# Kernel optimization log

Hardware: AMD Instinct MI355X
Metric: run time of the kernel (lower is better)

## Reference

```python
import jax, jax.numpy as jnp
import numpy as np

B, TK, H = 32, 1024, 512
N = 2 * H          # hidden_dim * 2
AD = 512           # attention_dimension


def setup_inputs() -> dict:
    key = jax.random.key(0)
    ks = jax.random.split(key, 11)
    s = 0.02  # weight scale
    return {
        's_t_hat': jax.random.normal(ks[0], (B, N), jnp.float32),
        'encoder_outputs': jax.random.normal(ks[1], (B, TK, N), jnp.float32),
        'encoder_feature': jax.random.normal(ks[2], (B * TK, N), jnp.float32),
        'enc_padding_mask': jax.random.uniform(ks[3], (B, TK), jnp.float32),
        'coverage': jax.random.uniform(ks[4], (B, TK), jnp.float32),
        'r_i': jax.random.normal(ks[5], (B, TK, AD), jnp.float32),
        'W_s_w': jax.random.normal(ks[6], (N, N), jnp.float32) * s,
        'W_s_b': jax.random.normal(ks[7], (N,), jnp.float32) * s,
        'W_c_w': jax.random.normal(ks[8], (N, 1), jnp.float32) * s,
        'v_w': jax.random.normal(ks[9], (1, N), jnp.float32) * s,
        'W_r_w': jax.random.normal(ks[10], (N, AD), jnp.float32) * s,
    }


def reference(s_t_hat, encoder_outputs, encoder_feature, enc_padding_mask,
              coverage, r_i, W_s_w, W_s_b, W_c_w, v_w, W_r_w):
    b, t_k, n = encoder_outputs.shape
    # decoder feature: W_s(s_t_hat), broadcast over time
    dec_fea = s_t_hat @ W_s_w.T + W_s_b                       # [b, n]
    enc_feat = encoder_feature.reshape(b, t_k, n)             # [b, t_k, n]
    # coverage feature: W_c applied to scalar coverage per position
    cov_feat = coverage[..., None] * W_c_w[:, 0]              # [b, t_k, n]
    e = jnp.tanh(enc_feat + dec_fea[:, None, :] + cov_feat)   # [b, t_k, n]
    scores = jnp.einsum('btn,n->bt', e, v_w[0])               # [b, t_k]
    attn_ = jax.nn.softmax(scores, axis=1) * enc_padding_mask
    attn = attn_ / attn_.sum(1, keepdims=True)                # renormalized
    c_t = jnp.einsum('bt,btn->bn', attn, encoder_outputs)     # [b, n]
    coverage_new = coverage + attn                            # [b, t_k]
    # structural (LSA) branch
    Wrri = jnp.einsum('bta,na->btn', r_i, W_r_w)              # [b, t_k, n]
    e_s = jnp.tanh(Wrri + dec_fea[:, None, :])
    s2 = jnp.einsum('btn,n->bt', e_s, v_w[0])
    a_struct = (jax.nn.softmax(s2, axis=1) * enc_padding_mask)[:, None, :]  # [b,1,t_k]
    c_t_struct = jnp.einsum('bt,btn->bn', a_struct[:, 0], encoder_outputs)  # [b, n]
    return (c_t, attn, coverage_new, c_t_struct, a_struct)
```

## Files before the change

### kernel.cpp

```cpp
#include <hip/hip_runtime.h>
#include <hip/hip_bf16.h>

static constexpr int BB   = 32;
static constexpr int TKK  = 1024;
static constexpr int ND   = 1024;
static constexpr int ADIM = 512;

typedef __attribute__((ext_vector_type(8))) short bf16x8;
typedef __attribute__((ext_vector_type(4))) float f32x4;

__device__ __forceinline__ float fast_tanh(float x) {
  x = fminf(fmaxf(x, -15.f), 15.f);
  float e = __expf(2.f * x);
  return __fdividef(e - 1.f, e + 1.f);
}

__device__ __forceinline__ short f2bf(float x) {
  unsigned u = __float_as_uint(x);
  u += 0x7FFF + ((u >> 16) & 1);
  return (short)(u >> 16);
}

__device__ __forceinline__ void gload_lds16(const void* g, void* l) {
  __builtin_amdgcn_global_load_lds(
      (const __attribute__((address_space(1))) unsigned int*)g,
      (__attribute__((address_space(3))) unsigned int*)l, 16, 0, 0);
}

__global__ __launch_bounds__(256) void k_cvt2(const float* __restrict__ r_i,
    const float* __restrict__ Wr, short* __restrict__ rb, short* __restrict__ wb) {
  size_t bid = blockIdx.x;
  const float* src;
  short* dst;
  size_t i;
  if (bid < 8192) { src = r_i; dst = rb; i = bid * 256 + threadIdx.x; }
  else            { src = Wr;  dst = wb; i = (bid - 8192) * 256 + threadIdx.x; }
  float4 a = ((const float4*)src)[2 * i];
  float4 b = ((const float4*)src)[2 * i + 1];
  bf16x8 h;
  h[0] = f2bf(a.x); h[1] = f2bf(a.y); h[2] = f2bf(a.z); h[3] = f2bf(a.w);
  h[4] = f2bf(b.x); h[5] = f2bf(b.y); h[6] = f2bf(b.z); h[7] = f2bf(b.w);
  ((bf16x8*)dst)[i] = h;
}

__global__ __launch_bounds__(256) void k_decfea(const float* __restrict__ s_t_hat,
    const float* __restrict__ Wsw, const float* __restrict__ Wsb,
    float* __restrict__ dec) {
  int b  = blockIdx.x >> 3;
  int n0 = (blockIdx.x & 7) << 7;
  int w = threadIdx.x >> 6, lane = threadIdx.x & 63;
  const float4* s4 = (const float4*)(s_t_hat + (size_t)b * ND);
  float4 sv0 = s4[lane], sv1 = s4[lane + 64], sv2 = s4[lane + 128], sv3 = s4[lane + 192];
  for (int nn = 0; nn < 32; nn++) {
    int n = n0 + w * 32 + nn;
    const float4* w4 = (const float4*)(Wsw + (size_t)n * ND);
    float4 wa = w4[lane], wb = w4[lane + 64], wc = w4[lane + 128], wd = w4[lane + 192];
    float acc = sv0.x*wa.x + sv0.y*wa.y + sv0.z*wa.z + sv0.w*wa.w
              + sv1.x*wb.x + sv1.y*wb.y + sv1.z*wb.z + sv1.w*wb.w
              + sv2.x*wc.x + sv2.y*wc.y + sv2.z*wc.z + sv2.w*wc.w
              + sv3.x*wd.x + sv3.y*wd.y + sv3.z*wd.z + sv3.w*wd.w;
    #pragma unroll
    for (int off = 32; off; off >>= 1) acc += __shfl_down(acc, off);
    if (lane == 0) dec[b * ND + n] = acc + Wsb[n];
  }
}

__global__ __launch_bounds__(256) void k_scoresA(const float* __restrict__ ef,
    const float* __restrict__ dec, const float* __restrict__ Wc,
    const float* __restrict__ vw, const float* __restrict__ cov,
    float* __restrict__ scores) {
  __shared__ float sb[4];
  int bt = blockIdx.x;
  int b  = bt >> 10;
  int tid = threadIdx.x;
  float4 e = *(const float4*)(ef + (size_t)bt * ND + tid * 4);
  float4 d = *(const float4*)(dec + (size_t)b * ND + tid * 4);
  float4 w = *(const float4*)(Wc + tid * 4);
  float4 v = *(const float4*)(vw + tid * 4);
  float c = cov[bt];
  float s = v.x * fast_tanh(e.x + d.x + c * w.x)
          + v.y * fast_tanh(e.y + d.y + c * w.y)
          + v.z * fast_tanh(e.z + d.z + c * w.z)
          + v.w * fast_tanh(e.w + d.w + c * w.w);
  #pragma unroll
  for (int off = 32; off; off >>= 1) s += __shfl_down(s, off);
  if ((tid & 63) == 0) sb[tid >> 6] = s;
  __syncthreads();
  if (tid == 0) scores[bt] = sb[0] + sb[1] + sb[2] + sb[3];
}

__global__ __launch_bounds__(256) void k_softmaxA(const float* __restrict__ scores,
    const float* __restrict__ mask, const float* __restrict__ cov,
    float* __restrict__ attn, float* __restrict__ covnew) {
  __shared__ float sb[4];
  int b = blockIdx.x, tid = threadIdx.x;
  float4 s = *(const float4*)(scores + (size_t)b * TKK + tid * 4);
  float m = fmaxf(fmaxf(s.x, s.y), fmaxf(s.z, s.w));
  #pragma unroll
  for (int off = 32; off; off >>= 1) m = fmaxf(m, __shfl_down(m, off));
  if ((tid & 63) == 0) sb[tid >> 6] = m;
  __syncthreads();
  m = fmaxf(fmaxf(sb[0], sb[1]), fmaxf(sb[2], sb[3]));
  float4 mk = *(const float4*)(mask + (size_t)b * TKK + tid * 4);
  float4 e;
  e.x = __expf(s.x - m) * mk.x;
  e.y = __expf(s.y - m) * mk.y;
  e.z = __expf(s.z - m) * mk.z;
  e.w = __expf(s.w - m) * mk.w;
  float sum = e.x + e.y + e.z + e.w;
  #pragma unroll
  for (int off = 32; off; off >>= 1) sum += __shfl_down(sum, off);
  __syncthreads();
  if ((tid & 63) == 0) sb[tid >> 6] = sum;
  __syncthreads();
  float inv = __fdividef(1.f, sb[0] + sb[1] + sb[2] + sb[3]);
  float4 a = {e.x * inv, e.y * inv, e.z * inv, e.w * inv};
  *(float4*)(attn + (size_t)b * TKK + tid * 4) = a;
  float4 c = *(const float4*)(cov + (size_t)b * TKK + tid * 4);
  float4 cn = {c.x + a.x, c.y + a.y, c.z + a.z, c.w + a.w};
  *(float4*)(covnew + (size_t)b * TKK + tid * 4) = cn;
}

__global__ __launch_bounds__(256) void k_gemmB3(const short* __restrict__ rb,
    const short* __restrict__ wb, const float* __restrict__ dec,
    const float* __restrict__ vw, float* __restrict__ part) {
  __shared__ __align__(16) short As[2][128 * 32];
  __shared__ __align__(16) short Bs[2][128 * 32];
  const int tid = threadIdx.x;
  const int lane = tid & 63, wv = tid >> 6;
  const int wm = wv >> 1, wn = wv & 1;
  const int g = lane >> 4, cl = lane & 15;
  const int mchunk = blockIdx.x, nchunk = blockIdx.y;
  const int b  = mchunk >> 3;
  const int t0 = (mchunk & 7) * 128;
  const int n0 = nchunk * 128;
  const int lrow4 = lane >> 2;
  const int sck   = ((lane & 3) ^ ((lane >> 3) & 3)) * 8;
  const short* Agbase = rb + (size_t)(b * TKK + t0) * ADIM;
  const short* Bgbase = wb + (size_t)n0 * ADIM;
  const int rdsw = (g ^ ((cl >> 1) & 3)) * 8;

  f32x4 acc[4][4];
  #pragma unroll
  for (int m = 0; m < 4; ++m)
    #pragma unroll
    for (int n = 0; n < 4; ++n) acc[m][n] = (f32x4){0.f, 0.f, 0.f, 0.f};

  auto stage = [&](int buf, int kc) {
    const int k0 = kc * 32;
    #pragma unroll
    for (int p = 0; p < 2; ++p) {
      const int rowc = p * 64 + wv * 16;
      const int row  = rowc + lrow4;
      gload_lds16(Agbase + (size_t)row * ADIM + k0 + sck, &As[buf][rowc * 32]);
      gload_lds16(Bgbase + (size_t)row * ADIM + k0 + sck, &Bs[buf][rowc * 32]);
    }
  };

  stage(0, 0);
  for (int kc = 0; kc < 16; ++kc) {
    const int cur = kc & 1;
    if (kc < 15) {
      stage(cur ^ 1, kc + 1);
      asm volatile("s_waitcnt vmcnt(4)" ::: "memory");
    } else {
      asm volatile("s_waitcnt vmcnt(0)" ::: "memory");
    }
    __builtin_amdgcn_s_barrier();
    bf16x8 af[4], bfr[4];
    #pragma unroll
    for (int m = 0; m < 4; ++m)
      af[m] = *(const bf16x8*)&As[cur][(wm * 64 + m * 16 + cl) * 32 + rdsw];
    #pragma unroll
    for (int n = 0; n < 4; ++n)
      bfr[n] = *(const bf16x8*)&Bs[cur][(wn * 64 + n * 16 + cl) * 32 + rdsw];
    #pragma unroll
    for (int m = 0; m < 4; ++m)
      #pragma unroll
      for (int n = 0; n < 4; ++n)
        acc[m][n] = __builtin_amdgcn_mfma_f32_16x16x32_bf16(af[m], bfr[n], acc[m][n], 0, 0, 0);
    __builtin_amdgcn_s_barrier();
  }

  float vvv[4], ddd[4];
  #pragma unroll
  for (int n = 0; n < 4; ++n) {
    const int col = n0 + wn * 64 + n * 16 + cl;
    vvv[n] = vw[col];
    ddd[n] = dec[b * ND + col];
  }
  #pragma unroll
  for (int m = 0; m < 4; ++m) {
    #pragma unroll
    for (int r = 0; r < 4; ++r) {
      float s = 0.f;
      #pragma unroll
      for (int n = 0; n < 4; ++n)
        s += vvv[n] * fast_tanh(acc[m][n][r] + ddd[n]);
      #pragma unroll
      for (int off = 1; off < 16; off <<= 1) s += __shfl_xor(s, off);
      if (cl == 0) {
        const int rowg = b * TKK + t0 + wm * 64 + m * 16 + g * 4 + r;
        part[(size_t)rowg * 16 + nchunk * 2 + wn] = s;
      }
    }
  }
}

__global__ __launch_bounds__(256) void k_gemmB(const float* __restrict__ r_i,
    const float* __restrict__ Wr, const float* __restrict__ dec,
    const float* __restrict__ vw, float* __restrict__ part) {
  __shared__ short As[128 * 64];
  __shared__ short Bs[128 * 64];
  const int tid = threadIdx.x;
  const int lane = tid & 63, wv = tid >> 6;
  const int wm = wv >> 1, wn = wv & 1;
  const int g = lane >> 4, cl = lane & 15;
  const int mchunk = blockIdx.x, nchunk = blockIdx.y;
  const int b  = mchunk >> 3;
  const int t0 = (mchunk & 7) * 128;
  const int n0 = nchunk * 128;
  const float* Ag = r_i + (size_t)(b * TKK + t0) * ADIM;
  const float* Bg = Wr + (size_t)n0 * ADIM;
  const int srow = tid >> 3, skk = (tid & 7) * 8;

  f32x4 acc[4][4];
  #pragma unroll
  for (int m = 0; m < 4; ++m)
    #pragma unroll
    for (int n = 0; n < 4; ++n) acc[m][n] = (f32x4){0.f, 0.f, 0.f, 0.f};

  for (int kc = 0; kc < 8; ++kc) {
    const int k0 = kc * 64;
    __syncthreads();
    #pragma unroll
    for (int dit = 0; dit < 4; ++dit) {
      const int row = dit * 32 + srow;
      const float* sa = Ag + (size_t)row * ADIM + k0 + skk;
      float4 a0 = *(const float4*)sa, a1 = *(const float4*)(sa + 4);
      bf16x8 ha;
      ha[0]=f2bf(a0.x); ha[1]=f2bf(a0.y); ha[2]=f2bf(a0.z); ha[3]=f2bf(a0.w);
      ha[4]=f2bf(a1.x); ha[5]=f2bf(a1.y); ha[6]=f2bf(a1.z); ha[7]=f2bf(a1.w);
      *(bf16x8*)&As[row * 64 + skk] = ha;
      const float* sbp = Bg + (size_t)row * ADIM + k0 + skk;
      float4 b0 = *(const float4*)sbp, b1 = *(const float4*)(sbp + 4);
      bf16x8 hb;
      hb[0]=f2bf(b0.x); hb[1]=f2bf(b0.y); hb[2]=f2bf(b0.z); hb[3]=f2bf(b0.w);
      hb[4]=f2bf(b1.x); hb[5]=f2bf(b1.y); hb[6]=f2bf(b1.z); hb[7]=f2bf(b1.w);
      *(bf16x8*)&Bs[row * 64 + skk] = hb;
    }
    __syncthreads();
    #pragma unroll
    for (int kf = 0; kf < 2; ++kf) {
      bf16x8 af[4], bfr[4];
      #pragma unroll
      for (int m = 0; m < 4; ++m)
        af[m] = *(const bf16x8*)&As[(wm * 64 + m * 16 + cl) * 64 + kf * 32 + g * 8];
      #pragma unroll
      for (int n = 0; n < 4; ++n)
        bfr[n] = *(const bf16x8*)&Bs[(wn * 64 + n * 16 + cl) * 64 + kf * 32 + g * 8];
      #pragma unroll
      for (int m = 0; m < 4; ++m)
        #pragma unroll
        for (int n = 0; n < 4; ++n)
          acc[m][n] = __builtin_amdgcn_mfma_f32_16x16x32_bf16(af[m], bfr[n], acc[m][n], 0, 0, 0);
    }
  }
  float vvv[4], ddd[4];
  #pragma unroll
  for (int n = 0; n < 4; ++n) {
    const int col = n0 + wn * 64 + n * 16 + cl;
    vvv[n] = vw[col];
    ddd[n] = dec[b * ND + col];
  }
  #pragma unroll
  for (int m = 0; m < 4; ++m) {
    #pragma unroll
    for (int r = 0; r < 4; ++r) {
      float s = 0.f;
      #pragma unroll
      for (int n = 0; n < 4; ++n)
        s += vvv[n] * fast_tanh(acc[m][n][r] + ddd[n]);
      #pragma unroll
      for (int off = 1; off < 16; off <<= 1) s += __shfl_xor(s, off);
      if (cl == 0) {
        const int rowg = b * TKK + t0 + wm * 64 + m * 16 + g * 4 + r;
        part[(size_t)rowg * 16 + nchunk * 2 + wn] = s;
      }
    }
  }
}

__global__ __launch_bounds__(256) void k_softmaxB(const float* __restrict__ part,
    const float* __restrict__ mask, float* __restrict__ astruct) {
  __shared__ float sb[4];
  int b = blockIdx.x, tid = threadIdx.x;
  float sv[4];
  #pragma unroll
  for (int tt = 0; tt < 4; ++tt) {
    const float4* pp = (const float4*)(part + ((size_t)b * TKK + tid * 4 + tt) * 16);
    float4 q0 = pp[0], q1 = pp[1], q2 = pp[2], q3 = pp[3];
    sv[tt] = q0.x+q0.y+q0.z+q0.w + q1.x+q1.y+q1.z+q1.w
           + q2.x+q2.y+q2.z+q2.w + q3.x+q3.y+q3.z+q3.w;
  }
  float m = fmaxf(fmaxf(sv[0], sv[1]), fmaxf(sv[2], sv[3]));
  #pragma unroll
  for (int off = 32; off; off >>= 1) m = fmaxf(m, __shfl_down(m, off));
  if ((tid & 63) == 0) sb[tid >> 6] = m;
  __syncthreads();
  m = fmaxf(fmaxf(sb[0], sb[1]), fmaxf(sb[2], sb[3]));
  float e0 = __expf(sv[0] - m), e1 = __expf(sv[1] - m);
  float e2 = __expf(sv[2] - m), e3 = __expf(sv[3] - m);
  float sum = e0 + e1 + e2 + e3;
  #pragma unroll
  for (int off = 32; off; off >>= 1) sum += __shfl_down(sum, off);
  __syncthreads();
  if ((tid & 63) == 0) sb[tid >> 6] = sum;
  __syncthreads();
  float inv = __fdividef(1.f, sb[0] + sb[1] + sb[2] + sb[3]);
  float4 mk = *(const float4*)(mask + (size_t)b * TKK + tid * 4);
  float4 a = {e0 * mk.x * inv, e1 * mk.y * inv, e2 * mk.z * inv, e3 * mk.w * inv};
  *(float4*)(astruct + (size_t)b * TKK + tid * 4) = a;
}

__global__ __launch_bounds__(256) void k_ctx(const float* __restrict__ enc,
    const float* __restrict__ attn, const float* __restrict__ astr,
    float* __restrict__ partials) {
  int tc = blockIdx.x, b = blockIdx.y;
  int tid = threadIdx.x, lane = tid & 63;
  float a1v = attn[(size_t)b * TKK + tc * 64 + lane];
  float a2v = astr[(size_t)b * TKK + tc * 64 + lane];
  const float4* e4 = (const float4*)(enc + (size_t)(b * TKK + tc * 64) * ND);
  float4 ac = {0, 0, 0, 0}, as = {0, 0, 0, 0};
  #pragma unroll 4
  for (int m = 0; m < 64; m++) {
    float a1 = __shfl(a1v, m), a2 = __shfl(a2v, m);
    float4 ev = e4[(size_t)m * 256 + tid];
    ac.x += a1 * ev.x; ac.y += a1 * ev.y; ac.z += a1 * ev.z; ac.w += a1 * ev.w;
    as.x += a2 * ev.x; as.y += a2 * ev.y; as.z += a2 * ev.z; as.w += a2 * ev.w;
  }
  float* p = partials + (size_t)(b * 16 + tc) * 2 * ND;
  *(float4*)(p + tid * 4) = ac;
  *(float4*)(p + ND + tid * 4) = as;
}

__global__ __launch_bounds__(256) void k_reduce(const float* __restrict__ partials,
    float* __restrict__ ct, float* __restrict__ cts) {
  int b = blockIdx.x, tid = threadIdx.x;
  float4 sc = {0, 0, 0, 0}, ss = {0, 0, 0, 0};
  for (int tc = 0; tc < 16; tc++) {
    const float* p = partials + (size_t)(b * 16 + tc) * 2 * ND;
    float4 p1 = *(const float4*)(p + tid * 4);
    float4 p2 = *(const float4*)(p + ND + tid * 4);
    sc.x += p1.x; sc.y += p1.y; sc.z += p1.z; sc.w += p1.w;
    ss.x += p2.x; ss.y += p2.y; ss.z += p2.z; ss.w += p2.w;
  }
  *(float4*)(ct + (size_t)b * ND + tid * 4) = sc;
  *(float4*)(cts + (size_t)b * ND + tid * 4) = ss;
}

extern "C" void kernel_launch(void* const* d_in, const int* in_sizes, int n_in,
                              void* d_out, int out_size, void* d_ws, size_t ws_size,
                              hipStream_t stream) {
  const float* s_t_hat = (const float*)d_in[0];
  const float* enc_out  = (const float*)d_in[1];
  const float* enc_feat = (const float*)d_in[2];
  const float* mask     = (const float*)d_in[3];
  const float* cov      = (const float*)d_in[4];
  const float* r_i      = (const float*)d_in[5];
  const float* Wsw      = (const float*)d_in[6];
  const float* Wsb      = (const float*)d_in[7];
  const float* Wc       = (const float*)d_in[8];
  const float* vw       = (const float*)d_in[9];
  const float* Wr       = (const float*)d_in[10];

  float* out    = (float*)d_out;
  float* ct     = out;
  float* attn   = out + 32768;
  float* covnew = out + 65536;
  float* cts    = out + 98304;
  float* astr   = out + 131072;

  float* ws       = (float*)d_ws;
  float* dec      = ws;
  float* scores   = ws + 32768;
  float* s2part   = ws + 65536;
  float* partials = ws + 589824;
  short* rb       = (short*)(ws + 1638400);
  short* wb       = rb + 16777216;
  const size_t NEEDED = 1638400ull * 4 + 16777216ull * 2 + 524288ull * 2;

  k_decfea<<<256, 256, 0, stream>>>(s_t_hat, Wsw, Wsb, dec);
  k_scoresA<<<BB * TKK, 256, 0, stream>>>(enc_feat, dec, Wc, vw, cov, scores);
  k_softmaxA<<<BB, 256, 0, stream>>>(scores, mask, cov, attn, covnew);
  if (ws_size >= NEEDED) {
    k_cvt2<<<8448, 256, 0, stream>>>(r_i, Wr, rb, wb);
    k_gemmB3<<<dim3(256, 8), 256, 0, stream>>>(rb, wb, dec, vw, s2part);
  } else {
    k_gemmB<<<dim3(256, 8), 256, 0, stream>>>(r_i, Wr, dec, vw, s2part);
  }
  k_softmaxB<<<BB, 256, 0, stream>>>(s2part, mask, astr);
  k_ctx<<<dim3(16, BB), 256, 0, stream>>>(enc_out, attn, astr, partials);
  k_reduce<<<BB, 256, 0, stream>>>(partials, ct, cts);
}
```

Baseline: 176.3 us.

## Restructure structural GEMM: full-K B tile in LDS, A streamed from global

Replaces the double-buffered 128x128 LDS-tiled bf16 GEMM with a 256x64 tile per 512-thread block. The whole 64xK weight slice is loaded once into swizzled LDS, and each wave reads its A rows straight from global memory into MFMA fragments. This removes the per-k-step barriers and A staging, and adds a block-index swizzle meant to improve L2 reuse. In exchange, A loads are uncoalesced 16-byte reads with no prefetch or overlap, and the 64KB of LDS per block limits occupancy.

```diff
diff --git a/kernel.cpp b/kernel.cpp
--- a/kernel.cpp
+++ b/kernel.cpp
@@ -121,87 +121,77 @@
   *(float4*)(covnew + (size_t)b * TKK + tid * 4) = cn;
 }
 
-__global__ __launch_bounds__(256) void k_gemmB3(const short* __restrict__ rb,
+__global__ __launch_bounds__(512, 4) void k_gemmB4(const short* __restrict__ rb,
     const short* __restrict__ wb, const float* __restrict__ dec,
     const float* __restrict__ vw, float* __restrict__ part) {
-  __shared__ __align__(16) short As[2][128 * 32];
-  __shared__ __align__(16) short Bs[2][128 * 32];
+  __shared__ __align__(16) short Bl[64 * ADIM];
   const int tid = threadIdx.x;
   const int lane = tid & 63, wv = tid >> 6;
-  const int wm = wv >> 1, wn = wv & 1;
   const int g = lane >> 4, cl = lane & 15;
-  const int mchunk = blockIdx.x, nchunk = blockIdx.y;
-  const int b  = mchunk >> 3;
-  const int t0 = (mchunk & 7) * 128;
-  const int n0 = nchunk * 128;
-  const int lrow4 = lane >> 2;
-  const int sck   = ((lane & 3) ^ ((lane >> 3) & 3)) * 8;
-  const short* Agbase = rb + (size_t)(b * TKK + t0) * ADIM;
-  const short* Bgbase = wb + (size_t)n0 * ADIM;
-  const int rdsw = (g ^ ((cl >> 1) & 3)) * 8;
-
-  f32x4 acc[4][4];
-  #pragma unroll
-  for (int m = 0; m < 4; ++m)
+  const int bid = blockIdx.x;
+  const int swz = (bid & 7) * 256 + (bid >> 3);
+  const int mchunk = swz >> 4, nchunk = swz & 15;
+  const int b  = mchunk >> 2;
+  const int t0 = (mchunk & 3) * 256;
+  const int n0 = nchunk * 64;
+  const short* Ag = rb + (size_t)(b * TKK + t0) * ADIM;
+  const short* Bg = wb + (size_t)n0 * ADIM;
+
+  #pragma unroll
+  for (int it = 0; it < 8; ++it) {
+    const int row = it * 8 + wv;
+    gload_lds16(Bg + (size_t)row * ADIM + (size_t)((lane ^ (row & 7)) * 8),
+                &Bl[row * ADIM]);
+  }
+  asm volatile("s_waitcnt vmcnt(0)" ::: "memory");
+  __builtin_amdgcn_s_barrier();
+
+  const int wrow = wv * 32;
+  const short* a0 = Ag + (size_t)(wrow + cl) * ADIM + g * 8;
+  const short* a1 = a0 + (size_t)16 * ADIM;
+
+  f32x4 acc[2][4];
+  #pragma unroll
+  for (int m = 0; m < 2; ++m)
     #pragma unroll
     for (int n = 0; n < 4; ++n) acc[m][n] = (f32x4){0.f, 0.f, 0.f, 0.f};
 
-  auto stage = [&](int buf, int kc) {
-    const int k0 = kc * 32;
-    #pragma unroll
-    for (int p = 0; p < 2; ++p) {
-      const int rowc = p * 64 + wv * 16;
-      const int row  = rowc + lrow4;
-      gload_lds16(Agbase + (size_t)row * ADIM + k0 + sck, &As[buf][rowc * 32]);
-      gload_lds16(Bgbase + (size_t)row * ADIM + k0 + sck, &Bs[buf][rowc * 32]);
-    }
-  };
-
-  stage(0, 0);
+  #pragma unroll
   for (int kc = 0; kc < 16; ++kc) {
-    const int cur = kc & 1;
-    if (kc < 15) {
-      stage(cur ^ 1, kc + 1);
-      asm volatile("s_waitcnt vmcnt(4)" ::: "memory");
-    } else {
-      asm volatile("s_waitcnt vmcnt(0)" ::: "memory");
-    }
-    __builtin_amdgcn_s_barrier();
-    bf16x8 af[4], bfr[4];
-    #pragma unroll
-    for (int m = 0; m < 4; ++m)
-      af[m] = *(const bf16x8*)&As[cur][(wm * 64 + m * 16 + cl) * 32 + rdsw];
+    bf16x8 af0 = *(const bf16x8*)(a0 + kc * 32);
+    bf16x8 af1 = *(const bf16x8*)(a1 + kc * 32);
+    bf16x8 bfr[4];
     #pragma unroll
     for (int n = 0; n < 4; ++n)
-      bfr[n] = *(const bf16x8*)&Bs[cur][(wn * 64 + n * 16 + cl) * 32 + rdsw];
-    #pragma unroll
-    for (int m = 0; m < 4; ++m)
-      #pragma unroll
-      for (int n = 0; n < 4; ++n)
-        acc[m][n] = __builtin_amdgcn_mfma_f32_16x16x32_bf16(af[m], bfr[n], acc[m][n], 0, 0, 0);
-    __builtin_amdgcn_s_barrier();
+      bfr[n] = *(const bf16x8*)&Bl[(n * 16 + cl) * ADIM
+                                   + (((kc * 4 + g) ^ (cl & 7)) * 8)];
+    #pragma unroll
+    for (int n = 0; n < 4; ++n) {
+      acc[0][n] = __builtin_amdgcn_mfma_f32_16x16x32_bf16(af0, bfr[n], acc[0][n], 0, 0, 0);
+      acc[1][n] = __builtin_amdgcn_mfma_f32_16x16x32_bf16(af1, bfr[n], acc[1][n], 0, 0, 0);
+    }
   }
 
   float vvv[4], ddd[4];
   #pragma unroll
   for (int n = 0; n < 4; ++n) {
-    const int col = n0 + wn * 64 + n * 16 + cl;
+    const int col = n0 + n * 16 + cl;
     vvv[n] = vw[col];
     ddd[n] = dec[b * ND + col];
   }
   #pragma unroll
-  for (int m = 0; m < 4; ++m) {
+  for (int mf = 0; mf < 2; ++mf) {
     #pragma unroll
     for (int r = 0; r < 4; ++r) {
       float s = 0.f;
       #pragma unroll
       for (int n = 0; n < 4; ++n)
-        s += vvv[n] * fast_tanh(acc[m][n][r] + ddd[n]);
+        s += vvv[n] * fast_tanh(acc[mf][n][r] + ddd[n]);
       #pragma unroll
       for (int off = 1; off < 16; off <<= 1) s += __shfl_xor(s, off);
       if (cl == 0) {
-        const int rowg = b * TKK + t0 + wm * 64 + m * 16 + g * 4 + r;
-        part[(size_t)rowg * 16 + nchunk * 2 + wn] = s;
+        const int rowg = b * TKK + t0 + wrow + mf * 16 + g * 4 + r;
+        part[(size_t)rowg * 16 + nchunk] = s;
       }
     }
   }
@@ -395,7 +385,7 @@
   k_softmaxA<<<BB, 256, 0, stream>>>(scores, mask, cov, attn, covnew);
   if (ws_size >= NEEDED) {
     k_cvt2<<<8448, 256, 0, stream>>>(r_i, Wr, rb, wb);
-    k_gemmB3<<<dim3(256, 8), 256, 0, stream>>>(rb, wb, dec, vw, s2part);
+    k_gemmB4<<<2048, 512, 0, stream>>>(rb, wb, dec, vw, s2part);
   } else {
     k_gemmB<<<dim3(256, 8), 256, 0, stream>>>(r_i, Wr, dec, vw, s2part);
   }
```

Result: slower. 190.4 us (+8.0%).
